# Kernel tuning notes

Hardware: AMD Instinct MI355X
Metric: run time of the kernel (lower is better)

Reference implementation:

```python
import jax, jax.numpy as jnp
import numpy as np

HEAD_DIM = 32
KERNEL = 3
DILATION = 2
SCALE = HEAD_DIM ** -0.5


def _unfold(x, kernel, dilation):
    # x: [B, C, H, W] -> patches [B, C, kernel*kernel, H, W]
    # matches nn.Unfold(kernel, dilation, padding=dilation*(kernel-1)//2, stride=1)
    B, C, H, W = x.shape
    pad = dilation * (kernel - 1) // 2
    xp = jnp.pad(x, ((0, 0), (0, 0), (pad, pad), (pad, pad)))
    patches = jnp.stack(
        [xp[:, :, i * dilation:i * dilation + H, j * dilation:j * dilation + W]
         for i in range(kernel) for j in range(kernel)],
        axis=2,
    )
    return patches  # [B, C, k*k, H, W]


def setup_inputs() -> dict:
    key = jax.random.key(0)
    kq, kk, kv = jax.random.split(key, 3)
    shape = (8, 192, 56, 56)
    return {
        "q": jax.random.normal(kq, shape, dtype=jnp.float32),
        "k": jax.random.normal(kk, shape, dtype=jnp.float32),
        "v": jax.random.normal(kv, shape, dtype=jnp.float32),
    }


def reference(q, k, v):
    B, d, H, W = q.shape
    h = d // HEAD_DIM
    kk2 = KERNEL * KERNEL
    HW = H * W

    # q: [B, h, hd, HW]
    qh = q.reshape(B, h, HEAD_DIM, HW)
    # unfolded k/v: [B, h, hd, k*k, HW]
    kp = _unfold(k, KERNEL, DILATION).reshape(B, h, HEAD_DIM, kk2, HW)
    vp = _unfold(v, KERNEL, DILATION).reshape(B, h, HEAD_DIM, kk2, HW)

    attn = jnp.einsum('bhdn,bhdkn->bhnk', qh, kp) * SCALE
    attn = jax.nn.softmax(attn, axis=-1)
    # dropout p=0 (eval): no-op

    # [B, h, HW, hd]
    out = jnp.einsum('bhnk,bhdkn->bhnd', attn, vp)
    # transpose(1,2).reshape(B,H,W,d): channel order = head-major
    out = out.transpose(0, 2, 1, 3).reshape(B, H, W, d)
    return out
```

## Files before the change

kernel.cpp:

```cpp
#include <hip/hip_runtime.h>

#define NH 6
#define HEAD_DIM 32
#define CCH 192
#define HH 56
#define WW 56
#define HWSZ (HH * WW)
#define KPOS 9
#define SCALE_LOG2E 0.25503486f
#define XPAD 61
#define ROWSZ (HEAD_DIM * XPAD)
#define JROWS 4
#define STRIPS 7

__device__ __forceinline__ float quad_xor1(float x) {
    return __int_as_float(
        __builtin_amdgcn_update_dpp(0, __float_as_int(x), 0xB1, 0xF, 0xF, true));
}
__device__ __forceinline__ float quad_xor2(float x) {
    return __int_as_float(
        __builtin_amdgcn_update_dpp(0, __float_as_int(x), 0x4E, 0xF, 0xF, true));
}

__global__ __launch_bounds__(256, 4) void dilate_attn_roll(
    const float* __restrict__ q,
    const float* __restrict__ k,
    const float* __restrict__ v,
    float* __restrict__ out)
{
    __shared__ float ks[3][ROWSZ];
    __shared__ float vs[3][ROWSZ];

    const int bh     = blockIdx.x % 48;
    const int ps     = blockIdx.x / 48;
    const int parity = ps / STRIPS;
    const int s      = ps % STRIPS;
    const int y0     = parity + 8 * s;
    const int t      = threadIdx.x;

    const size_t plane = (size_t)bh * HEAD_DIM * HWSZ;
    const int px = t >> 2;
    const int c  = t & 3;
    const bool active = px < WW;

    int sd[7], sx[7];
#pragma unroll
    for (int i = 0; i < 7; i++) {
        const int e = t + 256 * i;
        sd[i] = e / WW;
        sx[i] = e - sd[i] * WW;
    }

    float qcur[8];
    if (active) {
        const float* qb = q + plane + (size_t)(8 * c) * HWSZ + (size_t)y0 * WW + px;
#pragma unroll
        for (int j = 0; j < 8; j++) qcur[j] = qb[j * HWSZ];
    }

    for (int e = t; e < 3 * HEAD_DIM * 4; e += 256) {
        const int slot = e >> 7;
        const int rr   = e & 127;
        const int d    = rr >> 2;
        const int xc   = rr & 3;
        const int xp   = (xc < 2) ? xc : (56 + xc);
        ks[slot][d * XPAD + xp] = 0.0f;
        vs[slot][d * XPAD + xp] = 0.0f;
    }

    float kpre[7], vpre[7];
#pragma unroll
    for (int r = 0; r < 3; r++) {
        const int ky   = y0 - 2 + 2 * r;
        const bool okr = (ky >= 0) && (ky < HH);
#pragma unroll
        for (int i = 0; i < 7; i++) {
            const size_t g = plane + (size_t)sd[i] * HWSZ + (size_t)(okr ? ky : 0) * WW + sx[i];
            kpre[i] = okr ? k[g] : 0.0f;
            vpre[i] = okr ? v[g] : 0.0f;
        }
#pragma unroll
        for (int i = 0; i < 7; i++) {
            const int a = sd[i] * XPAD + sx[i] + 2;
            ks[r][a] = kpre[i];
            vs[r][a] = vpre[i];
        }
    }
    __syncthreads();

    float qnxt[8];
#pragma unroll
    for (int j = 0; j < JROWS; j++) {
        const int y = y0 + 2 * j;

        if (j < 3) {
            const int ky   = y0 + 4 + 2 * j;
            const bool okr = (ky < HH);
#pragma unroll
            for (int i = 0; i < 7; i++) {
                const size_t g = plane + (size_t)sd[i] * HWSZ + (size_t)(okr ? ky : 0) * WW + sx[i];
                kpre[i] = okr ? k[g] : 0.0f;
                vpre[i] = okr ? v[g] : 0.0f;
            }
            if (active) {
                const float* qb = q + plane + (size_t)(8 * c) * HWSZ + (size_t)(y + 2) * WW + px;
#pragma unroll
                for (int jj = 0; jj < 8; jj++) qnxt[jj] = qb[jj * HWSZ];
            }
        }

        if (active) {
            float lg[KPOS];
#pragma unroll
            for (int rp = 0; rp < 3; rp++) {
                const float* kr = &ks[(j + rp) % 3][(8 * c) * XPAD + px];
                float a0 = 0.f, a1 = 0.f, a2 = 0.f;
#pragma unroll
                for (int j8 = 0; j8 < 8; j8++) {
                    const float* p  = kr + j8 * XPAD;
                    const float qj = qcur[j8];
                    a0 = fmaf(qj, p[0], a0);
                    a1 = fmaf(qj, p[2], a1);
                    a2 = fmaf(qj, p[4], a2);
                }
                lg[3 * rp + 0] = a0;
                lg[3 * rp + 1] = a1;
                lg[3 * rp + 2] = a2;
            }
#pragma unroll
            for (int kk = 0; kk < KPOS; kk++) {
                float sm = lg[kk];
                sm += quad_xor1(sm);
                sm += quad_xor2(sm);
                lg[kk] = sm * SCALE_LOG2E;
            }
            const float m = fmaxf(fmaxf(fmaxf(lg[0], lg[1]), lg[2]),
                                  fmaxf(fmaxf(fmaxf(lg[3], lg[4]), lg[5]),
                                        fmaxf(fmaxf(lg[6], lg[7]), lg[8])));
            float ssum = 0.f;
#pragma unroll
            for (int kk = 0; kk < KPOS; kk++) {
                lg[kk] = exp2f(lg[kk] - m);
                ssum += lg[kk];
            }
            const float inv = __builtin_amdgcn_rcpf(ssum);

            float acc[8];
#pragma unroll
            for (int jj = 0; jj < 8; jj++) acc[jj] = 0.f;
#pragma unroll
            for (int rp = 0; rp < 3; rp++) {
                const float* vr = &vs[(j + rp) % 3][(8 * c) * XPAD + px];
                const float w0 = lg[3 * rp + 0];
                const float w1 = lg[3 * rp + 1];
                const float w2 = lg[3 * rp + 2];
#pragma unroll
                for (int jj = 0; jj < 8; jj++) {
                    const float* p = vr + jj * XPAD;
                    float a = acc[jj];
                    a = fmaf(w0, p[0], a);
                    a = fmaf(w1, p[2], a);
                    a = fmaf(w2, p[4], a);
                    acc[jj] = a;
                }
            }

            const int h = bh % NH;
            const int b = bh / NH;
            float* ob = out + ((size_t)((b * HH + y) * WW + px)) * CCH
                            + h * HEAD_DIM + 8 * c;
            reinterpret_cast<float4*>(ob)[0] =
                make_float4(acc[0] * inv, acc[1] * inv, acc[2] * inv, acc[3] * inv);
            reinterpret_cast<float4*>(ob)[1] =
                make_float4(acc[4] * inv, acc[5] * inv, acc[6] * inv, acc[7] * inv);
        }

        __syncthreads();

        if (j < 3) {
#pragma unroll
            for (int i = 0; i < 7; i++) {
                const int a = sd[i] * XPAD + sx[i] + 2;
                ks[j % 3][a] = kpre[i];
                vs[j % 3][a] = vpre[i];
            }
#pragma unroll
            for (int jj = 0; jj < 8; jj++) qcur[jj] = qnxt[jj];
        }

        __syncthreads();
    }
}

extern "C" void kernel_launch(void* const* d_in, const int* in_sizes, int n_in,
                              void* d_out, int out_size, void* d_ws, size_t ws_size,
                              hipStream_t stream) {
    const float* q = (const float*)d_in[0];
    const float* k = (const float*)d_in[1];
    const float* v = (const float*)d_in[2];
    float* out = (float*)d_out;

    const int blocks = 48 * 2 * STRIPS;
    dilate_attn_roll<<<blocks, 256, 0, stream>>>(q, k, v, out);
}
```

Before: 104.8 us.

## Store K/V tiles in LDS as packed fp16 pairs of neighbouring columns

K and V rows are converted to fp16 and stored in shared memory as packed pairs holding column x and column x+2, so each output's three dilated taps need two LDS reads instead of three. Global loads double because each thread also fetches the x+2 element, and the old zero-padding init of the halo is replaced by edge writes. This trades fewer LDS reads for extra global traffic and unpack/convert instructions, and reduces K/V precision to fp16 with round-toward-zero, which risks exceeding the accuracy tolerance.

```diff
diff --git a/kernel.cpp b/kernel.cpp
--- a/kernel.cpp
+++ b/kernel.cpp
@@ -13,6 +13,27 @@
 #define JROWS 4
 #define STRIPS 7
 
+typedef __fp16 h2_t __attribute__((ext_vector_type(2)));
+
+__device__ __forceinline__ unsigned pack_pair(float a, float b) {
+    h2_t h = __builtin_amdgcn_cvt_pkrtz(a, b);
+    unsigned u;
+    __builtin_memcpy(&u, &h, 4);
+    return u;
+}
+__device__ __forceinline__ float lo_f(unsigned u) {
+    unsigned short s = (unsigned short)(u & 0xffffu);
+    __fp16 h;
+    __builtin_memcpy(&h, &s, 2);
+    return (float)h;
+}
+__device__ __forceinline__ float hi_f(unsigned u) {
+    unsigned short s = (unsigned short)(u >> 16);
+    __fp16 h;
+    __builtin_memcpy(&h, &s, 2);
+    return (float)h;
+}
+
 __device__ __forceinline__ float quad_xor1(float x) {
     return __int_as_float(
         __builtin_amdgcn_update_dpp(0, __float_as_int(x), 0xB1, 0xF, 0xF, true));
@@ -22,14 +43,14 @@
         __builtin_amdgcn_update_dpp(0, __float_as_int(x), 0x4E, 0xF, 0xF, true));
 }
 
-__global__ __launch_bounds__(256, 4) void dilate_attn_roll(
+__global__ __launch_bounds__(256, 4) void dilate_attn_h2(
     const float* __restrict__ q,
     const float* __restrict__ k,
     const float* __restrict__ v,
     float* __restrict__ out)
 {
-    __shared__ float ks[3][ROWSZ];
-    __shared__ float vs[3][ROWSZ];
+    __shared__ unsigned ks[3][ROWSZ];
+    __shared__ unsigned vs[3][ROWSZ];
 
     const int bh     = blockIdx.x % 48;
     const int ps     = blockIdx.x / 48;
@@ -43,12 +64,17 @@
     const int c  = t & 3;
     const bool active = px < WW;
 
-    int sd[7], sx[7];
+    int gofs[7], sa[7];
+    unsigned edgemask = 0, okmask = 0;
 #pragma unroll
     for (int i = 0; i < 7; i++) {
         const int e = t + 256 * i;
-        sd[i] = e / WW;
-        sx[i] = e - sd[i] * WW;
+        const int d = e / WW;
+        const int x = e - d * WW;
+        gofs[i] = d * HWSZ + x;
+        sa[i]   = d * XPAD + x + 2;
+        if (x < 2)      edgemask |= 1u << i;
+        if (x + 2 < WW) okmask   |= 1u << i;
     }
 
     float qcur[8];
@@ -58,37 +84,35 @@
         for (int j = 0; j < 8; j++) qcur[j] = qb[j * HWSZ];
     }
 
-    for (int e = t; e < 3 * HEAD_DIM * 4; e += 256) {
-        const int slot = e >> 7;
-        const int rr   = e & 127;
-        const int d    = rr >> 2;
-        const int xc   = rr & 3;
-        const int xp   = (xc < 2) ? xc : (56 + xc);
-        ks[slot][d * XPAD + xp] = 0.0f;
-        vs[slot][d * XPAD + xp] = 0.0f;
-    }
-
-    float kpre[7], vpre[7];
 #pragma unroll
     for (int r = 0; r < 3; r++) {
         const int ky   = y0 - 2 + 2 * r;
         const bool okr = (ky >= 0) && (ky < HH);
+        const float* kb = k + plane + (size_t)(okr ? ky : 0) * WW;
+        const float* vb = v + plane + (size_t)(okr ? ky : 0) * WW;
+        float ka[7], kn[7], va[7], vn[7];
 #pragma unroll
         for (int i = 0; i < 7; i++) {
-            const size_t g = plane + (size_t)sd[i] * HWSZ + (size_t)(okr ? ky : 0) * WW + sx[i];
-            kpre[i] = okr ? k[g] : 0.0f;
-            vpre[i] = okr ? v[g] : 0.0f;
+            const bool ok2 = okr && ((okmask >> i) & 1);
+            ka[i] = okr ? kb[gofs[i]]     : 0.0f;
+            kn[i] = ok2 ? kb[gofs[i] + 2] : 0.0f;
+            va[i] = okr ? vb[gofs[i]]     : 0.0f;
+            vn[i] = ok2 ? vb[gofs[i] + 2] : 0.0f;
         }
 #pragma unroll
         for (int i = 0; i < 7; i++) {
-            const int a = sd[i] * XPAD + sx[i] + 2;
-            ks[r][a] = kpre[i];
-            vs[r][a] = vpre[i];
+            ks[r][sa[i]] = pack_pair(ka[i], kn[i]);
+            vs[r][sa[i]] = pack_pair(va[i], vn[i]);
+            if ((edgemask >> i) & 1) {
+                ks[r][sa[i] - 2] = pack_pair(0.0f, ka[i]);
+                vs[r][sa[i] - 2] = pack_pair(0.0f, va[i]);
+            }
         }
     }
     __syncthreads();
 
     float qnxt[8];
+    float kaN[7], knN[7], vaN[7], vnN[7];
 #pragma unroll
     for (int j = 0; j < JROWS; j++) {
         const int y = y0 + 2 * j;
@@ -96,11 +120,15 @@
         if (j < 3) {
             const int ky   = y0 + 4 + 2 * j;
             const bool okr = (ky < HH);
+            const float* kb = k + plane + (size_t)(okr ? ky : 0) * WW;
+            const float* vb = v + plane + (size_t)(okr ? ky : 0) * WW;
 #pragma unroll
             for (int i = 0; i < 7; i++) {
-                const size_t g = plane + (size_t)sd[i] * HWSZ + (size_t)(okr ? ky : 0) * WW + sx[i];
-                kpre[i] = okr ? k[g] : 0.0f;
-                vpre[i] = okr ? v[g] : 0.0f;
+                const bool ok2 = okr && ((okmask >> i) & 1);
+                kaN[i] = okr ? kb[gofs[i]]     : 0.0f;
+                knN[i] = ok2 ? kb[gofs[i] + 2] : 0.0f;
+                vaN[i] = okr ? vb[gofs[i]]     : 0.0f;
+                vnN[i] = ok2 ? vb[gofs[i] + 2] : 0.0f;
             }
             if (active) {
                 const float* qb = q + plane + (size_t)(8 * c) * HWSZ + (size_t)(y + 2) * WW + px;
@@ -113,15 +141,20 @@
             float lg[KPOS];
 #pragma unroll
             for (int rp = 0; rp < 3; rp++) {
-                const float* kr = &ks[(j + rp) % 3][(8 * c) * XPAD + px];
+                const unsigned* kr = &ks[(j + rp) % 3][(8 * c) * XPAD + px];
+                unsigned r0[8], r1[8];
+#pragma unroll
+                for (int j8 = 0; j8 < 8; j8++) {
+                    r0[j8] = kr[j8 * XPAD];
+                    r1[j8] = kr[j8 * XPAD + 2];
+                }
                 float a0 = 0.f, a1 = 0.f, a2 = 0.f;
 #pragma unroll
                 for (int j8 = 0; j8 < 8; j8++) {
-                    const float* p  = kr + j8 * XPAD;
                     const float qj = qcur[j8];
-                    a0 = fmaf(qj, p[0], a0);
-                    a1 = fmaf(qj, p[2], a1);
-                    a2 = fmaf(qj, p[4], a2);
+                    a0 = fmaf(qj, lo_f(r0[j8]), a0);
+                    a1 = fmaf(qj, hi_f(r0[j8]), a1);
+                    a2 = fmaf(qj, hi_f(r1[j8]), a2);
                 }
                 lg[3 * rp + 0] = a0;
                 lg[3 * rp + 1] = a1;
@@ -150,18 +183,23 @@
             for (int jj = 0; jj < 8; jj++) acc[jj] = 0.f;
 #pragma unroll
             for (int rp = 0; rp < 3; rp++) {
-                const float* vr = &vs[(j + rp) % 3][(8 * c) * XPAD + px];
+                const unsigned* vr = &vs[(j + rp) % 3][(8 * c) * XPAD + px];
+                unsigned r0[8], r1[8];
+#pragma unroll
+                for (int j8 = 0; j8 < 8; j8++) {
+                    r0[j8] = vr[j8 * XPAD];
+                    r1[j8] = vr[j8 * XPAD + 2];
+                }
                 const float w0 = lg[3 * rp + 0];
                 const float w1 = lg[3 * rp + 1];
                 const float w2 = lg[3 * rp + 2];
 #pragma unroll
-                for (int jj = 0; jj < 8; jj++) {
-                    const float* p = vr + jj * XPAD;
-                    float a = acc[jj];
-                    a = fmaf(w0, p[0], a);
-                    a = fmaf(w1, p[2], a);
-                    a = fmaf(w2, p[4], a);
-                    acc[jj] = a;
+                for (int j8 = 0; j8 < 8; j8++) {
+                    float a = acc[j8];
+                    a = fmaf(w0, lo_f(r0[j8]), a);
+                    a = fmaf(w1, hi_f(r0[j8]), a);
+                    a = fmaf(w2, hi_f(r1[j8]), a);
+                    acc[j8] = a;
                 }
             }
 
@@ -180,9 +218,12 @@
         if (j < 3) {
 #pragma unroll
             for (int i = 0; i < 7; i++) {
-                const int a = sd[i] * XPAD + sx[i] + 2;
-                ks[j % 3][a] = kpre[i];
-                vs[j % 3][a] = vpre[i];
+                ks[j % 3][sa[i]] = pack_pair(kaN[i], knN[i]);
+                vs[j % 3][sa[i]] = pack_pair(vaN[i], vnN[i]);
+                if ((edgemask >> i) & 1) {
+                    ks[j % 3][sa[i] - 2] = pack_pair(0.0f, kaN[i]);
+                    vs[j % 3][sa[i] - 2] = pack_pair(0.0f, vaN[i]);
+                }
             }
 #pragma unroll
             for (int jj = 0; jj < 8; jj++) qcur[jj] = qnxt[jj];
@@ -201,5 +242,5 @@
     float* out = (float*)d_out;
 
     const int blocks = 48 * 2 * STRIPS;
-    dilate_attn_roll<<<blocks, 256, 0, stream>>>(q, k, v, out);
-}
+    dilate_attn_h2<<<blocks, 256, 0, stream>>>(q, k, v, out);
+}
```

Result: slower. 107.6 us (+2.6%).
